# Optimization experiments

Measured on AMD Instinct MI355X. Metric: run time of the kernel, lower is better.

Reference implementation:

```python
import jax, jax.numpy as jnp
import numpy as np


def setup_inputs() -> dict:
    key = jax.random.key(0)
    k1, k2 = jax.random.split(key)
    n, c, h, w = 8, 2048, 64, 64
    out_c = 512
    fea = jax.random.normal(k1, (n, c, h, w), dtype=jnp.float32)
    # Conv2d weight [out, in, kh=1, kw=9]; kaiming-ish scale
    W = jax.random.normal(k2, (out_c, c, 1, 9), dtype=jnp.float32) * 0.02
    b = jnp.zeros((out_c,), dtype=jnp.float32)
    return {"fea": fea, "W": W, "b": b}


def reference(fea, W, b):
    # Original module (stride=1 path): for each width column i, take the
    # [n,c,h,1] slice, run Conv2d(kernel=(1,9), pad=(0,4)) + ReLU, concat on w.
    # For a width-1 input, only the CENTER kernel tap (kw index 4) overlaps
    # real data; all other taps see zero padding. Hence each column output is
    # ReLU(W[:,:,0,4] @ column + b), and the concat over columns is exactly a
    # pointwise (1x1) conv over the full feature map with the center tap.
    Wc = W[:, :, 0, 4]  # [out_c, in_c]
    out = jnp.einsum('nchw,oc->nohw', fea, Wc) + b[None, :, None, None]
    return jax.nn.relu(out)
```

## Files before the change

### kernel.cpp

```cpp
#include <hip/hip_runtime.h>
#include <hip/hip_bf16.h>

typedef __bf16 bf16x8 __attribute__((ext_vector_type(8)));
typedef float floatx4 __attribute__((ext_vector_type(4)));

#define KDIM 2048
#define MDIM 512
#define HWDIM 4096
#define BN 128
#define BM 256
#define BK 32
#define NITER (KDIM / BK)

__global__ void extract_w_kernel(const float* __restrict__ W, __bf16* __restrict__ Wc) {
  const int idx = blockIdx.x * 256 + threadIdx.x;
  const float4 v = ((const float4*)W)[idx];
  const float vv[4] = {v.x, v.y, v.z, v.w};
  const int f0 = idx * 4;
#pragma unroll
  for (int j = 0; j < 4; ++j) {
    const int f = f0 + j;
    if (f % 9 == 4) Wc[f / 9] = (__bf16)vv[j];
  }
}

__global__ __launch_bounds__(512, 4) void conv1x1_kernel(
    const float* __restrict__ fea, const __bf16* __restrict__ Wc,
    const float* __restrict__ bias, float* __restrict__ out) {
  __shared__ __align__(16) __bf16 Bs[2][BN * BK];

  const int t    = threadIdx.x;
  const int wave = t >> 6;
  const int lane = t & 63;
  const int l15  = lane & 15;
  const int quad = lane >> 4;

  const int xcd   = blockIdx.x & 7;
  const int slot  = blockIdx.x >> 3;
  const int tile  = xcd * 32 + (slot >> 1);
  const int mhalf = slot & 1;
  const int img   = tile >> 5;
  const int nb    = tile & 31;

  const int wm = mhalf * BM + wave * 32;

  const float* feaN = fea + (size_t)img * KDIM * HWDIM + (size_t)nb * BN;
  float*       outN = out + (size_t)img * MDIM * HWDIM + (size_t)nb * BN;

  const int hw   = lane + ((wave & 1) << 6);
  const int g    = wave >> 1;
  const int boff = hw * BK + (((g + (hw >> 1)) & 3) * 8);
  const float* bsrc = feaN + (size_t)g * 8 * HWDIM + hw;

  const __bf16* aptr = Wc + (size_t)(wm + l15) * KDIM + quad * 8;

  float bpf[2][8];
  floatx4 acc[2][8];
#pragma unroll
  for (int i = 0; i < 2; ++i)
#pragma unroll
    for (int j = 0; j < 8; ++j) acc[i][j] = (floatx4){0.f, 0.f, 0.f, 0.f};

#pragma unroll
  for (int j = 0; j < 8; ++j) bpf[0][j] = bsrc[(size_t)j * HWDIM];
#pragma unroll
  for (int j = 0; j < 8; ++j) bpf[1][j] = bsrc[(size_t)(BK + j) * HWDIM];
  {
    bf16x8 h0;
#pragma unroll
    for (int j = 0; j < 8; ++j) h0[j] = (__bf16)bpf[0][j];
    *(bf16x8*)&Bs[0][boff] = h0;
  }
  __syncthreads();

#define KBODY(I, CUR)                                                          \
  {                                                                            \
    const int i_ = (I);                                                        \
    bf16x8 af[2];                                                              \
    const __bf16* ap = aptr + (size_t)i_ * BK;                                 \
    _Pragma("unroll")                                                          \
    for (int mt = 0; mt < 2; ++mt)                                             \
      af[mt] = *(const bf16x8*)(ap + (size_t)(mt * 16) * KDIM);                \
    if (i_ + 1 < NITER) {                                                      \
      bf16x8 hn;                                                               \
      _Pragma("unroll")                                                        \
      for (int j = 0; j < 8; ++j) hn[j] = (__bf16)bpf[(CUR) ^ 1][j];           \
      *(bf16x8*)&Bs[(CUR) ^ 1][boff] = hn;                                     \
    }                                                                          \
    if (i_ + 2 < NITER) {                                                      \
      const float* p = bsrc + (size_t)(i_ + 2) * BK * HWDIM;                   \
      _Pragma("unroll")                                                        \
      for (int j = 0; j < 8; ++j) bpf[(CUR)][j] = p[(size_t)j * HWDIM];        \
    }                                                                          \
    _Pragma("unroll")                                                          \
    for (int nt = 0; nt < 8; ++nt) {                                           \
      const int n_ = nt * 16 + l15;                                            \
      const bf16x8 bfr = *(const bf16x8*)&Bs[(CUR)][n_ * BK +                  \
                            (((quad + (n_ >> 1)) & 3) * 8)];                   \
      _Pragma("unroll")                                                        \
      for (int mt = 0; mt < 2; ++mt)                                           \
        acc[mt][nt] = __builtin_amdgcn_mfma_f32_16x16x32_bf16(af[mt], bfr,     \
                          acc[mt][nt], 0, 0, 0);                               \
    }                                                                          \
    __syncthreads();                                                           \
  }

  for (int i = 0; i < NITER; i += 2) {
    KBODY(i, 0)
    KBODY(i + 1, 1)
  }
#undef KBODY

#pragma unroll
  for (int mt = 0; mt < 2; ++mt) {
    const int o0 = wm + mt * 16 + quad * 4;
    const float4 bv = *(const float4*)(bias + o0);
    const float bvr[4] = {bv.x, bv.y, bv.z, bv.w};
#pragma unroll
    for (int r = 0; r < 4; ++r) {
      const size_t ro = (size_t)(o0 + r) * HWDIM;
#pragma unroll
      for (int nt = 0; nt < 8; ++nt) {
        float x = acc[mt][nt][r] + bvr[r];
        x = x > 0.f ? x : 0.f;
        __builtin_nontemporal_store(x, &outN[ro + nt * 16 + l15]);
      }
    }
  }
}

extern "C" void kernel_launch(void* const* d_in, const int* in_sizes, int n_in,
                              void* d_out, int out_size, void* d_ws, size_t ws_size,
                              hipStream_t stream) {
  const float* fea  = (const float*)d_in[0];
  const float* W    = (const float*)d_in[1];
  const float* bias = (const float*)d_in[2];
  float* out = (float*)d_out;
  __bf16* Wc = (__bf16*)d_ws;

  hipLaunchKernelGGL(extract_w_kernel, dim3(9216), dim3(256), 0, stream, W, Wc);
  hipLaunchKernelGGL(conv1x1_kernel, dim3(512), dim3(512), 0, stream, fea, Wc, bias, out);
}
```

Baseline: 437.4 us.

## Split output channels into four quarter-tiles with 256-thread blocks

Measured after the change: 473.8 us. 8.3% more time.

```diff
diff --git a/kernel.cpp b/kernel.cpp
--- a/kernel.cpp
+++ b/kernel.cpp
@@ -8,7 +8,7 @@
 #define MDIM 512
 #define HWDIM 4096
 #define BN 128
-#define BM 256
+#define BM 128
 #define BK 32
 #define NITER (KDIM / BK)
 
@@ -24,7 +24,7 @@
   }
 }
 
-__global__ __launch_bounds__(512, 4) void conv1x1_kernel(
+__global__ __launch_bounds__(256, 4) void conv1x1_kernel(
     const float* __restrict__ fea, const __bf16* __restrict__ Wc,
     const float* __restrict__ bias, float* __restrict__ out) {
   __shared__ __align__(16) __bf16 Bs[2][BN * BK];
@@ -35,26 +35,28 @@
   const int l15  = lane & 15;
   const int quad = lane >> 4;
 
-  const int xcd   = blockIdx.x & 7;
-  const int slot  = blockIdx.x >> 3;
-  const int tile  = xcd * 32 + (slot >> 1);
-  const int mhalf = slot & 1;
-  const int img   = tile >> 5;
-  const int nb    = tile & 31;
+  const int xcd  = blockIdx.x & 7;
+  const int slot = blockIdx.x >> 3;
+  const int tile = xcd * 32 + (slot >> 2);
+  const int mq   = slot & 3;
+  const int img  = tile >> 5;
+  const int nb   = tile & 31;
 
-  const int wm = mhalf * BM + wave * 32;
+  const int wm = mq * BM + wave * 32;
 
   const float* feaN = fea + (size_t)img * KDIM * HWDIM + (size_t)nb * BN;
   float*       outN = out + (size_t)img * MDIM * HWDIM + (size_t)nb * BN;
 
-  const int hw   = lane + ((wave & 1) << 6);
-  const int g    = wave >> 1;
-  const int boff = hw * BK + (((g + (hw >> 1)) & 3) * 8);
-  const float* bsrc = feaN + (size_t)g * 8 * HWDIM + hw;
+  const int hw = t & 127;
+  const int kg = t >> 7;
+  const int b0 = hw * BK + (((kg     + (hw >> 1)) & 3) * 8);
+  const int b1 = hw * BK + (((2 + kg + (hw >> 1)) & 3) * 8);
+  const float* src0 = feaN + (size_t)(kg * 8) * HWDIM + hw;
+  const float* src1 = feaN + (size_t)(16 + kg * 8) * HWDIM + hw;
 
   const __bf16* aptr = Wc + (size_t)(wm + l15) * KDIM + quad * 8;
 
-  float bpf[2][8];
+  float pfa[8], pfb[8];
   floatx4 acc[2][8];
 #pragma unroll
   for (int i = 0; i < 2; ++i)
@@ -62,15 +64,22 @@
     for (int j = 0; j < 8; ++j) acc[i][j] = (floatx4){0.f, 0.f, 0.f, 0.f};
 
 #pragma unroll
-  for (int j = 0; j < 8; ++j) bpf[0][j] = bsrc[(size_t)j * HWDIM];
+  for (int j = 0; j < 8; ++j) pfa[j] = src0[(size_t)j * HWDIM];
 #pragma unroll
-  for (int j = 0; j < 8; ++j) bpf[1][j] = bsrc[(size_t)(BK + j) * HWDIM];
+  for (int j = 0; j < 8; ++j) pfb[j] = src1[(size_t)j * HWDIM];
   {
-    bf16x8 h0;
+    bf16x8 h0, h1;
 #pragma unroll
-    for (int j = 0; j < 8; ++j) h0[j] = (__bf16)bpf[0][j];
-    *(bf16x8*)&Bs[0][boff] = h0;
+    for (int j = 0; j < 8; ++j) h0[j] = (__bf16)pfa[j];
+#pragma unroll
+    for (int j = 0; j < 8; ++j) h1[j] = (__bf16)pfb[j];
+    *(bf16x8*)&Bs[0][b0] = h0;
+    *(bf16x8*)&Bs[0][b1] = h1;
   }
+#pragma unroll
+  for (int j = 0; j < 8; ++j) pfa[j] = src0[(size_t)(BK + j) * HWDIM];
+#pragma unroll
+  for (int j = 0; j < 8; ++j) pfb[j] = src1[(size_t)(BK + j) * HWDIM];
   __syncthreads();
 
 #define KBODY(I, CUR)                                                          \
@@ -84,13 +93,24 @@
     if (i_ + 1 < NITER) {                                                      \
       bf16x8 hn;                                                               \
       _Pragma("unroll")                                                        \
-      for (int j = 0; j < 8; ++j) hn[j] = (__bf16)bpf[(CUR) ^ 1][j];           \
-      *(bf16x8*)&Bs[(CUR) ^ 1][boff] = hn;                                     \
+      for (int j = 0; j < 8; ++j) hn[j] = (__bf16)pfa[j];                      \
+      *(bf16x8*)&Bs[(CUR) ^ 1][b0] = hn;                                       \
     }                                                                          \
     if (i_ + 2 < NITER) {                                                      \
-      const float* p = bsrc + (size_t)(i_ + 2) * BK * HWDIM;                   \
+      const float* p = src0 + (size_t)(i_ + 2) * BK * HWDIM;                   \
       _Pragma("unroll")                                                        \
-      for (int j = 0; j < 8; ++j) bpf[(CUR)][j] = p[(size_t)j * HWDIM];        \
+      for (int j = 0; j < 8; ++j) pfa[j] = p[(size_t)j * HWDIM];               \
+    }                                                                          \
+    if (i_ + 1 < NITER) {                                                      \
+      bf16x8 hn;                                                               \
+      _Pragma("unroll")                                                        \
+      for (int j = 0; j < 8; ++j) hn[j] = (__bf16)pfb[j];                      \
+      *(bf16x8*)&Bs[(CUR) ^ 1][b1] = hn;                                       \
+    }                                                                          \
+    if (i_ + 2 < NITER) {                                                      \
+      const float* p = src1 + (size_t)(i_ + 2) * BK * HWDIM;                   \
+      _Pragma("unroll")                                                        \
+      for (int j = 0; j < 8; ++j) pfb[j] = p[(size_t)j * HWDIM];               \
     }                                                                          \
     _Pragma("unroll")                                                          \
     for (int nt = 0; nt < 8; ++nt) {                                           \
@@ -139,5 +159,5 @@
   __bf16* Wc = (__bf16*)d_ws;
 
   hipLaunchKernelGGL(extract_w_kernel, dim3(9216), dim3(256), 0, stream, W, Wc);
-  hipLaunchKernelGGL(conv1x1_kernel, dim3(512), dim3(512), 0, stream, fea, Wc, bias, out);
+  hipLaunchKernelGGL(conv1x1_kernel, dim3(1024), dim3(256), 0, stream, fea, Wc, bias, out);
 }
```
